# Performance work log

Hardware: AMD Instinct MI355X
Metric: run time of the kernel (lower is better)

The kernel has to match this reference:

```python
import jax, jax.numpy as jnp
import numpy as np
import math

D_MODEL = 512
DIM_K = 512
DIM_V = 512
N_HEADS = 8


def setup_inputs() -> dict:
    key = jax.random.key(0)
    ks = jax.random.split(key, 12)
    B, S = 2, 2048
    sc = 1.0 / math.sqrt(D_MODEL)
    return {
        "x": jax.random.normal(ks[0], (B, S, D_MODEL), dtype=jnp.float32),
        "y": jax.random.normal(ks[1], (B, S, D_MODEL), dtype=jnp.float32),
        # weights stored [in, out] so linear is x @ W + b
        "Wq": jax.random.normal(ks[2], (D_MODEL, DIM_K), dtype=jnp.float32) * sc,
        "bq": jnp.zeros((DIM_K,), dtype=jnp.float32),
        "Wk": jax.random.normal(ks[3], (D_MODEL, DIM_K), dtype=jnp.float32) * sc,
        "bk": jnp.zeros((DIM_K,), dtype=jnp.float32),
        "Wv": jax.random.normal(ks[4], (D_MODEL, DIM_V), dtype=jnp.float32) * sc,
        "bv": jnp.zeros((DIM_V,), dtype=jnp.float32),
        "Wo": jax.random.normal(ks[5], (DIM_V, D_MODEL), dtype=jnp.float32) * sc,
        "bo": jnp.zeros((D_MODEL,), dtype=jnp.float32),
    }


def reference(x, y, Wq, bq, Wk, bk, Wv, bv, Wo, bo):
    B, S, _ = x.shape
    H = N_HEADS
    Dh = DIM_K // H
    Dvh = DIM_V // H
    norm = 1.0 / math.sqrt(D_MODEL)  # note: original scales by 1/sqrt(d_model)

    # torch: q(x).reshape(-1, B, S, Dh) -> heads on leading dim (row-major)
    Q = (x @ Wq + bq).reshape(-1, B, S, Dh)      # [H,B,S,Dh]
    K = (y @ Wk + bk).reshape(-1, B, S, Dh)      # [H,B,S,Dh]
    V = (y @ Wv + bv).reshape(-1, B, S, Dvh)     # [H,B,S,Dvh]

    scores = jnp.einsum('hbqd,hbkd->hbqk', Q, K) * norm  # [H,B,S,S]

    # median-threshold mask: torch.median on even n returns lower middle value
    med_idx = (S - 1) // 2
    thre = jnp.sort(scores, axis=-1)[..., med_idx:med_idx + 1]  # [H,B,S,1]
    masked = scores - thre <= 0  # mask where score <= median
    scores = jnp.where(masked, -jnp.inf, scores)

    attn = jax.nn.softmax(scores, axis=-1)
    # dropout omitted (deterministic / eval mode)
    out = jnp.einsum('hbqk,hbkd->hbqd', attn, V)  # [H,B,S,Dvh]
    out = out.reshape(B, S, -1)                   # faithful row-major reshape
    return out @ Wo + bo
```

## Files before the change

### kernel.cpp

```cpp
#include <hip/hip_runtime.h>
#include <hip/hip_bf16.h>
#include <stdint.h>

#define SEQ    2048
#define DMODEL 512
#define NPANEL 16
#define NORM   0.044194173824159216f

typedef _Float16 f16;
typedef __attribute__((ext_vector_type(8))) _Float16 half8;
typedef __attribute__((ext_vector_type(2))) _Float16 half2v;
typedef __attribute__((ext_vector_type(4))) float f32x4;
typedef __attribute__((ext_vector_type(4))) unsigned int u32x4;

__device__ __forceinline__ unsigned umin2(unsigned a, unsigned b){ return a<b?a:b; }
__device__ __forceinline__ unsigned umax2(unsigned a, unsigned b){ return a>b?a:b; }

__global__ __launch_bounds__(256) void k_cvt(const float4* __restrict__ x,
                                             const float4* __restrict__ y,
                                             f16* __restrict__ xh, f16* __restrict__ xl,
                                             f16* __restrict__ yh, f16* __restrict__ yl){
  int i = blockIdx.x*256 + threadIdx.x;
  float4 a = x[i]; float4 b = y[i];
  half2v h0 = {(f16)a.x, (f16)a.y}, h1 = {(f16)a.z, (f16)a.w};
  *(half2v*)(xh + i*4)     = h0; *(half2v*)(xh + i*4 + 2) = h1;
  half2v l0 = {(f16)(a.x-(float)h0[0]), (f16)(a.y-(float)h0[1])};
  half2v l1 = {(f16)(a.z-(float)h1[0]), (f16)(a.w-(float)h1[1])};
  *(half2v*)(xl + i*4)     = l0; *(half2v*)(xl + i*4 + 2) = l1;
  half2v g0 = {(f16)b.x, (f16)b.y}, g1 = {(f16)b.z, (f16)b.w};
  *(half2v*)(yh + i*4)     = g0; *(half2v*)(yh + i*4 + 2) = g1;
  half2v m0 = {(f16)(b.x-(float)g0[0]), (f16)(b.y-(float)g0[1])};
  half2v m1 = {(f16)(b.z-(float)g1[0]), (f16)(b.w-(float)g1[1])};
  *(half2v*)(yl + i*4)     = m0; *(half2v*)(yl + i*4 + 2) = m1;
}

__global__ __launch_bounds__(256) void k_wt(const float* __restrict__ Wq, const float* __restrict__ Wk,
                                            const float* __restrict__ Wv, const float* __restrict__ Wo,
                                            f16* __restrict__ Wth, f16* __restrict__ Wtl){
  int z = blockIdx.z;
  const float* W = (z==0)?Wq:(z==1)?Wk:(z==2)?Wv:Wo;
  __shared__ float tile[64][65];
  int k0 = blockIdx.x*64, n0 = blockIdx.y*64;
  #pragma unroll
  for (int i = 0; i < 16; ++i){
    int s = threadIdx.x + i*256; int kl2 = s>>6, nl = s&63;
    tile[kl2][nl] = W[(k0+kl2)*512 + (n0+nl)];
  }
  __syncthreads();
  #pragma unroll
  for (int i = 0; i < 16; ++i){
    int s = threadIdx.x + i*256; int nl = s>>6, kl2 = s&63;
    float v = tile[kl2][nl];
    f16 h = (f16)v;
    int idx = z*262144 + (n0+nl)*512 + (k0+kl2);
    Wth[idx] = h;
    Wtl[idx] = (f16)(v - (float)h);
  }
}

template<int FINAL>
__global__ __launch_bounds__(256) void k_gemm(const f16* __restrict__ Ah0, const f16* __restrict__ Al0,
                                              const f16* __restrict__ Ah1, const f16* __restrict__ Al1,
                                              const f16* __restrict__ Wh, const f16* __restrict__ Wl,
                                              const float* __restrict__ b0, const float* __restrict__ b1,
                                              const float* __restrict__ b2,
                                              f16* __restrict__ Oq, float* __restrict__ Of){
  int z = blockIdx.z;
  const f16* A  = (z==0) ? Ah0 : Ah1;
  const f16* Alp= (z==0) ? Al0 : Al1;
  const f16* Bh = Wh + z*262144;
  const f16* Bl = Wl + z*262144;
  const float* bias = (z==0)?b0:(z==1)?b1:b2;
  const bool split = (FINAL==0) && (z<2);
  int m0 = blockIdx.x*128, n0 = blockIdx.y*128;

  __shared__ f16 Ahs[128][40], Bhs[128][40], Als[128][40], Bls[128][40];

  int t = threadIdx.x, l = t&63, w = t>>6;
  int wr = w>>1, wc = w&1;
  int lr = l&15, lk = l>>4;

  f32x4 acc[4][4];
  #pragma unroll
  for (int i=0;i<4;++i)
    #pragma unroll
    for (int j=0;j<4;++j) acc[i][j] = (f32x4){0.f,0.f,0.f,0.f};

  for (int ks = 0; ks < 16; ++ks){
    int k0 = ks*32;
    #pragma unroll
    for (int i = 0; i < 2; ++i){
      int s = t + i*256; int r = s>>2, kc = s&3;
      *(u32x4*)(&Ahs[r][kc*8]) = *(const u32x4*)(A   + (m0+r)*512 + k0 + kc*8);
      *(u32x4*)(&Bhs[r][kc*8]) = *(const u32x4*)(Bh  + (n0+r)*512 + k0 + kc*8);
      if (split){
        *(u32x4*)(&Als[r][kc*8]) = *(const u32x4*)(Alp + (m0+r)*512 + k0 + kc*8);
        *(u32x4*)(&Bls[r][kc*8]) = *(const u32x4*)(Bl  + (n0+r)*512 + k0 + kc*8);
      }
    }
    __syncthreads();
    half8 ah[4], bh2[4], al2[4], bl2[4];
    #pragma unroll
    for (int tm = 0; tm < 4; ++tm) ah[tm]  = *(const half8*)(&Ahs[wr*64 + tm*16 + lr][lk*8]);
    #pragma unroll
    for (int tn = 0; tn < 4; ++tn) bh2[tn] = *(const half8*)(&Bhs[wc*64 + tn*16 + lr][lk*8]);
    if (split){
      #pragma unroll
      for (int tm = 0; tm < 4; ++tm) al2[tm] = *(const half8*)(&Als[wr*64 + tm*16 + lr][lk*8]);
      #pragma unroll
      for (int tn = 0; tn < 4; ++tn) bl2[tn] = *(const half8*)(&Bls[wc*64 + tn*16 + lr][lk*8]);
    }
    #pragma unroll
    for (int tm = 0; tm < 4; ++tm)
      #pragma unroll
      for (int tn = 0; tn < 4; ++tn){
        acc[tm][tn] = __builtin_amdgcn_mfma_f32_16x16x32_f16(ah[tm], bh2[tn], acc[tm][tn], 0,0,0);
        if (split){
          acc[tm][tn] = __builtin_amdgcn_mfma_f32_16x16x32_f16(ah[tm], bl2[tn], acc[tm][tn], 0,0,0);
          acc[tm][tn] = __builtin_amdgcn_mfma_f32_16x16x32_f16(al2[tm], bh2[tn], acc[tm][tn], 0,0,0);
        }
      }
    __syncthreads();
  }

  #pragma unroll
  for (int tn = 0; tn < 4; ++tn){
    int n_g = n0 + wc*64 + tn*16 + lr;
    float bv = bias[n_g];
    #pragma unroll
    for (int tm = 0; tm < 4; ++tm){
      #pragma unroll
      for (int r = 0; r < 4; ++r){
        int m_g = m0 + wr*64 + tm*16 + lk*4 + r;
        float v = acc[tm][tn][r] + bv;
        size_t idx = (size_t)m_g*512 + n_g;
        if (FINAL){
          Of[idx] = v;
        } else if (z < 2){
          f16 h = (f16)v;
          Oq[(size_t)z*4194304 + idx] = h;
          Oq[(size_t)z*4194304 + 2097152 + idx] = (f16)(v - (float)h);
        } else {
          Oq[(size_t)4*2097152 + idx] = (f16)v;
        }
      }
    }
  }
}

__global__ __launch_bounds__(256) void k_vt(const unsigned short* __restrict__ V, unsigned short* __restrict__ Vt){
  int p = blockIdx.y;
  int t = threadIdx.x;
  int d = t & 63, sc = t >> 6;
  int s0b = blockIdx.x*32 + sc*8;
  const unsigned short* Vp = V + p*131072;
  unsigned short* Vtp = Vt + p*131072;
  typedef __attribute__((ext_vector_type(8))) short short8;
  short8 vv;
  #pragma unroll
  for (int j = 0; j < 8; ++j) vv[j] = (short)Vp[(s0b + j)*64 + d];
  *(short8*)(Vtp + d*2048 + s0b) = vv;
}

__global__ __launch_bounds__(1024, 8) void k_attn(const f16* __restrict__ Qh, const f16* __restrict__ Ql,
                                                  const f16* __restrict__ Kh, const f16* __restrict__ Kl,
                                                  const f16* __restrict__ Vt, f16* __restrict__ O){
  extern __shared__ char scb[];
  __shared__ float red[3072];
  __shared__ float rzs[16];
  int p = blockIdx.y, qt = blockIdx.x;
  int s0 = qt*16;
  const f16* Qhp = Qh + p*131072;
  const f16* Qlp = Ql + p*131072;
  const f16* Khp = Kh + p*131072;
  const f16* Klp = Kl + p*131072;
  const f16* Vtp = Vt + p*131072;
  int t = threadIdx.x, l = t&63, w = t>>6;
  int lr = l&15, lk = l>>4;

  half8 qh[2], qlo[2];
  #pragma unroll
  for (int f = 0; f < 2; ++f){
    qh[f]  = *(const half8*)(Qhp + (s0+lr)*64 + f*32 + lk*8);
    qlo[f] = *(const half8*)(Qlp + (s0+lr)*64 + f*32 + lk*8);
  }

  unsigned oA[16], oB[16];
  #pragma unroll
  for (int ph = 0; ph < 2; ++ph){
    #pragma unroll
    for (int ct = 0; ct < 4; ++ct){
      int ng = ph*1024 + w*64 + ct*16 + lr;
      const f16* kb = Khp + ng*64 + lk*8;
      const f16* lb = Klp + ng*64 + lk*8;
      half8 kh0 = *(const half8*)(kb);
      half8 kh1 = *(const half8*)(kb + 32);
      f32x4 c = (f32x4){0.f,0.f,0.f,0.f};
      c = __builtin_amdgcn_mfma_f32_16x16x32_f16(qh[0],  kh0, c, 0,0,0);
      c = __builtin_amdgcn_mfma_f32_16x16x32_f16(qh[1],  kh1, c, 0,0,0);
      c = __builtin_amdgcn_mfma_f32_16x16x32_f16(qlo[0], kh0, c, 0,0,0);
      c = __builtin_amdgcn_mfma_f32_16x16x32_f16(qlo[1], kh1, c, 0,0,0);
      half8 kl0 = *(const half8*)(lb);
      half8 kl1 = *(const half8*)(lb + 32);
      c = __builtin_amdgcn_mfma_f32_16x16x32_f16(qh[0],  kl0, c, 0,0,0);
      c = __builtin_amdgcn_mfma_f32_16x16x32_f16(qh[1],  kl1, c, 0,0,0);
      #pragma unroll
      for (int r = 0; r < 4; ++r){
        int row = lk*4 + r;
        int n = w*64 + ct*16 + lr;
        *(float*)(scb + row*4096 + (((unsigned)(n*4)) ^ ((unsigned)(lk<<6)))) = c[r];
      }
    }
    __syncthreads();
    {
      unsigned C = ((unsigned)((w>>2)&3))<<6;
      const char* rb = scb + w*4096;
      #pragma unroll
      for (int j = 0; j < 16; ++j){
        unsigned u = *(const unsigned*)(rb + (((unsigned)((l + j*64)*4)) ^ C));
        unsigned e = ((int)u < 0) ? ~u : (u | 0x80000000u);
        if (ph == 0) oA[j] = e; else oB[j] = e;
      }
    }
    if (ph == 0) __syncthreads();
  }

  {
    unsigned umn = 0xFFFFFFFFu, umx = 0u;
    #pragma unroll
    for (int j = 0; j < 16; ++j){
      umn = umin2(umn, umin2(oA[j], oB[j]));
      umx = umax2(umax2(umx, oA[j]), oB[j]);
    }
    #pragma unroll
    for (int off2 = 1; off2 < 64; off2 <<= 1){
      umn = umin2(umn, (unsigned)__shfl_xor((int)umn, off2));
      umx = umax2(umx, (unsigned)__shfl_xor((int)umx, off2));
    }
    unsigned thr;
    {
      unsigned L = umn, R = umx;
      #pragma unroll 1
      for (;;){
        if (L >= R){ thr = R; break; }
        unsigned mid = L + ((R - L) >> 1);
        int c = 0;
        #pragma unroll
        for (int j = 0; j < 16; ++j){
          c += (int)__popcll(__ballot(oA[j] <= mid));
          c += (int)__popcll(__ballot(oB[j] <= mid));
        }
        if (c == 1024){ thr = mid; break; }
        if (c > 1024) R = mid; else L = mid + 1;
      }
    }
    unsigned bmx = (umx & 0x80000000u) ? (umx & 0x7FFFFFFFu) : ~umx;
    float mx = __uint_as_float(bmx);
    float zs = 0.f;
    unsigned g = ((unsigned)(w & 7)) << 4;
    char* pb = scb + w*4096;
    #pragma unroll
    for (int j = 0; j < 32; ++j){
      unsigned a = (j < 16) ? oA[j] : oB[j-16];
      unsigned b = (a & 0x80000000u) ? (a & 0x7FFFFFFFu) : ~a;
      float v = __uint_as_float(b);
      float wgt = (a <= thr) ? 0.f : __expf((v - mx) * NORM);
      zs += wgt;
      unsigned col = (unsigned)((j & 15)*64 + l + (j >> 4)*1024);
      *(f16*)(pb + ((col*2) ^ g)) = (f16)wgt;
    }
    #pragma unroll
    for (int off2 = 1; off2 < 64; off2 <<= 1) zs += __shfl_xor(zs, off2);
    if (l == 0) rzs[w] = 1.f / zs;
  }
  __syncthreads();

  int oc = w & 3, kh = w >> 2;
  const f16* vbase = Vtp + (oc*16 + lr)*2048 + kh*512 + lk*8;
  const char* pbase = scb + lr*4096;
  unsigned pswz = ((unsigned)(lr & 7)) << 4;
  f32x4 o0 = (f32x4){0.f,0.f,0.f,0.f};
  f32x4 o1 = (f32x4){0.f,0.f,0.f,0.f};
  #pragma unroll
  for (int kc = 0; kc < 16; ++kc){
    half8 pa = *(const half8*)(pbase + (((unsigned)((kh*512 + kc*32 + lk*8)*2)) ^ pswz));
    half8 vb = *(const half8*)(vbase + kc*32);
    if (kc & 1) o1 = __builtin_amdgcn_mfma_f32_16x16x32_f16(pa, vb, o1, 0,0,0);
    else        o0 = __builtin_amdgcn_mfma_f32_16x16x32_f16(pa, vb, o0, 0,0,0);
  }
  f32x4 oa;
  #pragma unroll
  for (int r = 0; r < 4; ++r) oa[r] = o0[r] + o1[r];
  if (kh > 0){
    #pragma unroll
    for (int r = 0; r < 4; ++r) red[(kh-1)*1024 + (lk*4+r)*64 + oc*16 + lr] = oa[r];
  }
  __syncthreads();
  if (kh == 0){
    #pragma unroll
    for (int r = 0; r < 4; ++r){
      int row = lk*4 + r;
      int cидx = row*64 + oc*16 + lr;
      float v = (oa[r] + red[cидx] + red[1024 + cидx] + red[2048 + cидx]) * rzs[row];
      O[p*131072 + (s0+row)*64 + oc*16 + lr] = (f16)v;
    }
  }
}

extern "C" void kernel_launch(void* const* d_in, const int* in_sizes, int n_in,
                              void* d_out, int out_size, void* d_ws, size_t ws_size,
                              hipStream_t stream) {
  const float* x  = (const float*)d_in[0];
  const float* y  = (const float*)d_in[1];
  const float* Wq = (const float*)d_in[2];
  const float* bq = (const float*)d_in[3];
  const float* Wk = (const float*)d_in[4];
  const float* bk = (const float*)d_in[5];
  const float* Wv = (const float*)d_in[6];
  const float* bv = (const float*)d_in[7];
  const float* Wo = (const float*)d_in[8];
  const float* bo = (const float*)d_in[9];

  f16* ws = (f16*)d_ws;
  f16* xh  = ws;
  f16* xl  = ws + 2097152;
  f16* yh  = ws + 4194304;
  f16* yl  = ws + 6291456;
  f16* Wth = ws + 8388608;
  f16* Wtl = ws + 9437184;
  f16* QKV = ws + 10485760;
  f16* Vt  = ws;
  f16* Ob  = ws + 2097152;

  (void)hipFuncSetAttribute(reinterpret_cast<const void*>(k_attn),
                            hipFuncAttributeMaxDynamicSharedMemorySize, 65536);

  k_cvt<<<2048, 256, 0, stream>>>((const float4*)x, (const float4*)y, xh, xl, yh, yl);
  k_wt<<<dim3(8,8,4), 256, 0, stream>>>(Wq, Wk, Wv, Wo, Wth, Wtl);
  k_gemm<0><<<dim3(32,4,3), 256, 0, stream>>>(xh, xl, yh, yl, Wth, Wtl, bq, bk, bv, QKV, nullptr);
  k_vt<<<dim3(64,16), 256, 0, stream>>>((const unsigned short*)(QKV + 4*2097152), (unsigned short*)Vt);
  k_attn<<<dim3(128,16), 1024, 65536, stream>>>(QKV, QKV + 2097152, QKV + 2*2097152, QKV + 3*2097152, Vt, Ob);
  k_gemm<1><<<dim3(32,4,1), 256, 0, stream>>>(Ob, Ob, Ob, Ob, Wth + 3*262144, Wtl, bo, bo, bo, nullptr, (float*)d_out);
}
```

Measured before the change: 306.2 us.

## Shrink attention blocks to 8 query rows and 512 threads

The attention kernel now handles 8 query rows per block with 8 waves instead of 16 rows with 16 waves. Grid axes are swapped so panels vary fastest, which may improve K/V cache reuse across neighbouring blocks. LDS use is halved so more blocks can be resident per CU, and the PV reduction is cut from four partial sums to two. In exchange, half of each 16-row MFMA tile is wasted (rows duplicated via qr=lr&7), so matrix-core work per output row roughly doubles, and each wave counts twice as many key columns.

```diff
diff --git a/kernel.cpp b/kernel.cpp
--- a/kernel.cpp
+++ b/kernel.cpp
@@ -162,14 +162,14 @@
   *(short8*)(Vtp + d*2048 + s0b) = vv;
 }
 
-__global__ __launch_bounds__(1024, 8) void k_attn(const f16* __restrict__ Qh, const f16* __restrict__ Ql,
-                                                  const f16* __restrict__ Kh, const f16* __restrict__ Kl,
-                                                  const f16* __restrict__ Vt, f16* __restrict__ O){
+__global__ __launch_bounds__(512, 8) void k_attn(const f16* __restrict__ Qh, const f16* __restrict__ Ql,
+                                                 const f16* __restrict__ Kh, const f16* __restrict__ Kl,
+                                                 const f16* __restrict__ Vt, f16* __restrict__ O){
   extern __shared__ char scb[];
-  __shared__ float red[3072];
-  __shared__ float rzs[16];
-  int p = blockIdx.y, qt = blockIdx.x;
-  int s0 = qt*16;
+  __shared__ float red[512];
+  __shared__ float rzs[8];
+  int p = blockIdx.x, qt = blockIdx.y;
+  int s0 = qt*8;
   const f16* Qhp = Qh + p*131072;
   const f16* Qlp = Ql + p*131072;
   const f16* Khp = Kh + p*131072;
@@ -177,38 +177,41 @@
   const f16* Vtp = Vt + p*131072;
   int t = threadIdx.x, l = t&63, w = t>>6;
   int lr = l&15, lk = l>>4;
+  int qr = lr & 7;
 
   half8 qh[2], qlo[2];
   #pragma unroll
   for (int f = 0; f < 2; ++f){
-    qh[f]  = *(const half8*)(Qhp + (s0+lr)*64 + f*32 + lk*8);
-    qlo[f] = *(const half8*)(Qlp + (s0+lr)*64 + f*32 + lk*8);
+    qh[f]  = *(const half8*)(Qhp + (s0+qr)*64 + f*32 + lk*8);
+    qlo[f] = *(const half8*)(Qlp + (s0+qr)*64 + f*32 + lk*8);
   }
 
   unsigned oA[16], oB[16];
-  #pragma unroll
+  #pragma unroll 1
   for (int ph = 0; ph < 2; ++ph){
-    #pragma unroll
-    for (int ct = 0; ct < 4; ++ct){
-      int ng = ph*1024 + w*64 + ct*16 + lr;
+    #pragma unroll 2
+    for (int ct = 0; ct < 8; ++ct){
+      int ng = ph*1024 + w*128 + ct*16 + lr;
       const f16* kb = Khp + ng*64 + lk*8;
       const f16* lb = Klp + ng*64 + lk*8;
       half8 kh0 = *(const half8*)(kb);
       half8 kh1 = *(const half8*)(kb + 32);
+      half8 kl0 = *(const half8*)(lb);
+      half8 kl1 = *(const half8*)(lb + 32);
       f32x4 c = (f32x4){0.f,0.f,0.f,0.f};
       c = __builtin_amdgcn_mfma_f32_16x16x32_f16(qh[0],  kh0, c, 0,0,0);
       c = __builtin_amdgcn_mfma_f32_16x16x32_f16(qh[1],  kh1, c, 0,0,0);
       c = __builtin_amdgcn_mfma_f32_16x16x32_f16(qlo[0], kh0, c, 0,0,0);
       c = __builtin_amdgcn_mfma_f32_16x16x32_f16(qlo[1], kh1, c, 0,0,0);
-      half8 kl0 = *(const half8*)(lb);
-      half8 kl1 = *(const half8*)(lb + 32);
       c = __builtin_amdgcn_mfma_f32_16x16x32_f16(qh[0],  kl0, c, 0,0,0);
       c = __builtin_amdgcn_mfma_f32_16x16x32_f16(qh[1],  kl1, c, 0,0,0);
-      #pragma unroll
-      for (int r = 0; r < 4; ++r){
-        int row = lk*4 + r;
-        int n = w*64 + ct*16 + lr;
-        *(float*)(scb + row*4096 + (((unsigned)(n*4)) ^ ((unsigned)(lk<<6)))) = c[r];
+      if (lk < 2){
+        #pragma unroll
+        for (int r = 0; r < 4; ++r){
+          int row = lk*4 + r;
+          int n = w*128 + ct*16 + lr;
+          *(float*)(scb + row*4096 + (((unsigned)(n*4)) ^ ((unsigned)(lk<<6)))) = c[r];
+        }
       }
     }
     __syncthreads();
@@ -222,7 +225,7 @@
         if (ph == 0) oA[j] = e; else oB[j] = e;
       }
     }
-    if (ph == 0) __syncthreads();
+    __syncthreads();
   }
 
   {
@@ -257,7 +260,7 @@
     unsigned bmx = (umx & 0x80000000u) ? (umx & 0x7FFFFFFFu) : ~umx;
     float mx = __uint_as_float(bmx);
     float zs = 0.f;
-    unsigned g = ((unsigned)(w & 7)) << 4;
+    unsigned g = ((unsigned)w) << 4;
     char* pb = scb + w*4096;
     #pragma unroll
     for (int j = 0; j < 32; ++j){
@@ -276,14 +279,14 @@
   __syncthreads();
 
   int oc = w & 3, kh = w >> 2;
-  const f16* vbase = Vtp + (oc*16 + lr)*2048 + kh*512 + lk*8;
-  const char* pbase = scb + lr*4096;
-  unsigned pswz = ((unsigned)(lr & 7)) << 4;
+  const f16* vbase = Vtp + (oc*16 + lr)*2048 + kh*1024 + lk*8;
+  const char* pbase = scb + qr*4096;
+  unsigned pswz = ((unsigned)qr) << 4;
   f32x4 o0 = (f32x4){0.f,0.f,0.f,0.f};
   f32x4 o1 = (f32x4){0.f,0.f,0.f,0.f};
-  #pragma unroll
-  for (int kc = 0; kc < 16; ++kc){
-    half8 pa = *(const half8*)(pbase + (((unsigned)((kh*512 + kc*32 + lk*8)*2)) ^ pswz));
+  #pragma unroll 4
+  for (int kc = 0; kc < 32; ++kc){
+    half8 pa = *(const half8*)(pbase + (((unsigned)((kh*1024 + kc*32 + lk*8)*2)) ^ pswz));
     half8 vb = *(const half8*)(vbase + kc*32);
     if (kc & 1) o1 = __builtin_amdgcn_mfma_f32_16x16x32_f16(pa, vb, o1, 0,0,0);
     else        o0 = __builtin_amdgcn_mfma_f32_16x16x32_f16(pa, vb, o0, 0,0,0);
@@ -291,17 +294,16 @@
   f32x4 oa;
   #pragma unroll
   for (int r = 0; r < 4; ++r) oa[r] = o0[r] + o1[r];
-  if (kh > 0){
-    #pragma unroll
-    for (int r = 0; r < 4; ++r) red[(kh-1)*1024 + (lk*4+r)*64 + oc*16 + lr] = oa[r];
+  if (kh == 1 && lk < 2){
+    #pragma unroll
+    for (int r = 0; r < 4; ++r) red[oc*128 + (lk*4+r)*16 + lr] = oa[r];
   }
   __syncthreads();
-  if (kh == 0){
+  if (kh == 0 && lk < 2){
     #pragma unroll
     for (int r = 0; r < 4; ++r){
       int row = lk*4 + r;
-      int cидx = row*64 + oc*16 + lr;
-      float v = (oa[r] + red[cидx] + red[1024 + cидx] + red[2048 + cидx]) * rzs[row];
+      float v = (oa[r] + red[oc*128 + row*16 + lr]) * rzs[row];
       O[p*131072 + (s0+row)*64 + oc*16 + lr] = (f16)v;
     }
   }
@@ -333,12 +335,12 @@
   f16* Ob  = ws + 2097152;
 
   (void)hipFuncSetAttribute(reinterpret_cast<const void*>(k_attn),
-                            hipFuncAttributeMaxDynamicSharedMemorySize, 65536);
+                            hipFuncAttributeMaxDynamicSharedMemorySize, 32768);
 
   k_cvt<<<2048, 256, 0, stream>>>((const float4*)x, (const float4*)y, xh, xl, yh, yl);
   k_wt<<<dim3(8,8,4), 256, 0, stream>>>(Wq, Wk, Wv, Wo, Wth, Wtl);
   k_gemm<0><<<dim3(32,4,3), 256, 0, stream>>>(xh, xl, yh, yl, Wth, Wtl, bq, bk, bv, QKV, nullptr);
   k_vt<<<dim3(64,16), 256, 0, stream>>>((const unsigned short*)(QKV + 4*2097152), (unsigned short*)Vt);
-  k_attn<<<dim3(128,16), 1024, 65536, stream>>>(QKV, QKV + 2097152, QKV + 2*2097152, QKV + 3*2097152, Vt, Ob);
+  k_attn<<<dim3(16,256), 512, 32768, stream>>>(QKV, QKV + 2097152, QKV + 2*2097152, QKV + 3*2097152, Vt, Ob);
   k_gemm<1><<<dim3(32,4,1), 256, 0, stream>>>(Ob, Ob, Ob, Ob, Wth + 3*262144, Wtl, bo, bo, bo, nullptr, (float*)d_out);
 }
```

After: 493.4 us. 1.61x slower.
